# Performance work log

Measured on AMD Instinct MI355X. Metric: run time of the kernel, lower is better.

The kernel has to match this reference:

```python
import jax, jax.numpy as jnp
import numpy as np

N = 50000      # nodes
E = 600000     # edges (avg degree 12)
D_IN = 32      # Processor hard-codes first GBlock in_channels=32
D_H = 128      # args.d_hidden
N_MID = 3      # n_mp - 1 = layers after the first (2 skip + 1 no-skip)


def setup_inputs() -> dict:
    key = jax.random.key(0)
    ks = jax.random.split(key, 10)
    s_in = 1.0 / np.sqrt(D_IN)
    s_h = 1.0 / np.sqrt(D_H)
    return {
        "z": jax.random.normal(ks[0], (N, D_IN), jnp.float32),
        "edge_index": jax.random.randint(ks[1], (2, E), 0, N, dtype=jnp.int32),
        "edge_weight": jax.random.uniform(ks[2], (E,), jnp.float32),
        "batch": jnp.zeros((N,), jnp.int32),
        # first GBlock (32 -> 128)
        "W_rel0": jax.random.normal(ks[3], (D_H, D_IN), jnp.float32) * s_in,
        "b_rel0": jax.random.normal(ks[4], (D_H,), jnp.float32) * 0.01,
        "W_root0": jax.random.normal(ks[5], (D_H, D_IN), jnp.float32) * s_in,
        # remaining 3 GBlocks (128 -> 128), stacked
        "W_rel": jax.random.normal(ks[6], (N_MID, D_H, D_H), jnp.float32) * s_h,
        "b_rel": jax.random.normal(ks[7], (N_MID, D_H), jnp.float32) * 0.01,
        "W_root": jax.random.normal(ks[8], (N_MID, D_H, D_H), jnp.float32) * s_h,
    }


def graph_conv(x, src, dst, w, W_rel, b_rel, W_root):
    # PyG GraphConv: lin_rel(sum_{j->i} w_e * x_j) + lin_root(x)
    msg = x[src] * w[:, None]                                   # [E, d] gather
    agg = jax.ops.segment_sum(msg, dst, num_segments=x.shape[0])  # [N, d] scatter-add
    return agg @ W_rel.T + b_rel + x @ W_root.T


def reference(z, edge_index, edge_weight, batch, W_rel0, b_rel0, W_root0, W_rel, b_rel, W_root):
    src, dst = edge_index[0], edge_index[1]
    # GBlock 0: 32 -> 128, norm=Identity, no skip
    out = jax.nn.relu(graph_conv(z, src, dst, edge_weight, W_rel0, b_rel0, W_root0))
    # GBlocks 1..2 with residual+relu, GBlock 3 without
    skips = (True, True, False)
    for i, skip in enumerate(skips):
        h = jax.nn.relu(graph_conv(out, src, dst, edge_weight, W_rel[i], b_rel[i], W_root[i]))
        out = jax.nn.relu(h + out) if skip else h
    # dropout with p=0.0 (eval) is identity
    return out
```

## Files before the change

### kernel.cpp

```cpp
#include <hip/hip_runtime.h>

#define N_NODES 50000
#define N_EDGES 600000
#define D_IN 32
#define D_H 128
#define CAP 64

typedef __attribute__((ext_vector_type(8))) short short8;
typedef __attribute__((ext_vector_type(4))) float f32x4;

static inline int cdiv(int a, int b) { return (a + b - 1) / b; }

__device__ inline unsigned short f2bf(float f) {
    unsigned int b = __float_as_uint(f);
    return (unsigned short)((b + 0x7FFFu + ((b >> 16) & 1u)) >> 16);
}
__device__ inline unsigned int pack_bf16(float a, float b) {
    return (unsigned int)f2bf(a) | ((unsigned int)f2bf(b) << 16);
}
__device__ inline float bf_lo(unsigned int u) { return __uint_as_float(u << 16); }
__device__ inline float bf_hi(unsigned int u) { return __uint_as_float(u & 0xFFFF0000u); }


__global__ __launch_bounds__(256) void prep_kernel(
    const float* __restrict__ z, unsigned int* __restrict__ zbf,
    const float* __restrict__ Wrel0, const float* __restrict__ Wroot0,
    const float* __restrict__ Wrel, const float* __restrict__ Wroot,
    unsigned short* __restrict__ W0, unsigned short* __restrict__ W1,
    int* __restrict__ cnt) {
    int i = blockIdx.x * 256 + threadIdx.x;
    if (i < N_NODES) cnt[i] = 0;
    if (i < N_NODES * D_IN / 4) {
        float4 v = ((const float4*)z)[i];
        ((uint2*)zbf)[i] = make_uint2(pack_bf16(v.x, v.y), pack_bf16(v.z, v.w));
    }
    if (i < 128 * 64) {
        int o = i >> 6, k = i & 63;
        float v = (k < 32) ? Wrel0[o * 32 + k] : Wroot0[o * 32 + (k - 32)];
        W0[i] = f2bf(v);
    }
    if (i < 3 * 128 * 256) {
        int L = i >> 15;
        int r = i & 32767;
        int o = r >> 8, k = r & 255;
        float v = (k < 128) ? Wrel[L * 16384 + o * 128 + k]
                            : Wroot[L * 16384 + o * 128 + (k - 128)];
        W1[i] = f2bf(v);
    }
}


__global__ void fillpad_kernel(const int* __restrict__ src, const int* __restrict__ dst,
                               const float* __restrict__ w, int* __restrict__ cnt,
                               int2* __restrict__ ep, int e) {
    int i = blockIdx.x * blockDim.x + threadIdx.x;
    if (i < e) {
        int d = dst[i];
        int slot = atomicAdd(&cnt[d], 1);
        if (slot < CAP) ep[(size_t)d * CAP + slot] = make_int2(src[i], __float_as_int(w[i]));
    }
}


__global__ __launch_bounds__(256) void agg128_kernel(
    const unsigned int* __restrict__ xbf, const int* __restrict__ cnt,
    const int2* __restrict__ ep, unsigned int* __restrict__ aggbf, int n) {
    int tid = threadIdx.x;
    int wid = tid >> 6, l = tid & 63;
    int sub = l >> 4, q = l & 15;
    int node = blockIdx.x * 16 + wid * 4 + sub;
    if (node >= n) return;
    int deg = cnt[node]; if (deg > CAP) deg = CAP;
    const uint4* X4 = (const uint4*)xbf;
    const unsigned long long* row = (const unsigned long long*)(ep + (size_t)node * CAP);
    float a0 = 0.f, a1 = 0.f, a2 = 0.f, a3 = 0.f, a4 = 0.f, a5 = 0.f, a6 = 0.f, a7 = 0.f;
    int j = 0;
    for (; j + 4 <= deg; j += 4) {
        unsigned long long e0 = __builtin_nontemporal_load(row + j);
        unsigned long long e1 = __builtin_nontemporal_load(row + j + 1);
        unsigned long long e2 = __builtin_nontemporal_load(row + j + 2);
        unsigned long long e3 = __builtin_nontemporal_load(row + j + 3);
        uint4 v0 = X4[(size_t)(unsigned int)e0 * 16 + q];
        uint4 v1 = X4[(size_t)(unsigned int)e1 * 16 + q];
        uint4 v2 = X4[(size_t)(unsigned int)e2 * 16 + q];
        uint4 v3 = X4[(size_t)(unsigned int)e3 * 16 + q];
        float w0 = __uint_as_float((unsigned int)(e0 >> 32));
        float w1 = __uint_as_float((unsigned int)(e1 >> 32));
        float w2 = __uint_as_float((unsigned int)(e2 >> 32));
        float w3 = __uint_as_float((unsigned int)(e3 >> 32));
        a0 += bf_lo(v0.x) * w0; a1 += bf_hi(v0.x) * w0; a2 += bf_lo(v0.y) * w0; a3 += bf_hi(v0.y) * w0;
        a4 += bf_lo(v0.z) * w0; a5 += bf_hi(v0.z) * w0; a6 += bf_lo(v0.w) * w0; a7 += bf_hi(v0.w) * w0;
        a0 += bf_lo(v1.x) * w1; a1 += bf_hi(v1.x) * w1; a2 += bf_lo(v1.y) * w1; a3 += bf_hi(v1.y) * w1;
        a4 += bf_lo(v1.z) * w1; a5 += bf_hi(v1.z) * w1; a6 += bf_lo(v1.w) * w1; a7 += bf_hi(v1.w) * w1;
        a0 += bf_lo(v2.x) * w2; a1 += bf_hi(v2.x) * w2; a2 += bf_lo(v2.y) * w2; a3 += bf_hi(v2.y) * w2;
        a4 += bf_lo(v2.z) * w2; a5 += bf_hi(v2.z) * w2; a6 += bf_lo(v2.w) * w2; a7 += bf_hi(v2.w) * w2;
        a0 += bf_lo(v3.x) * w3; a1 += bf_hi(v3.x) * w3; a2 += bf_lo(v3.y) * w3; a3 += bf_hi(v3.y) * w3;
        a4 += bf_lo(v3.z) * w3; a5 += bf_hi(v3.z) * w3; a6 += bf_lo(v3.w) * w3; a7 += bf_hi(v3.w) * w3;
    }
    for (; j < deg; j++) {
        unsigned long long e0 = __builtin_nontemporal_load(row + j);
        uint4 v0 = X4[(size_t)(unsigned int)e0 * 16 + q];
        float w0 = __uint_as_float((unsigned int)(e0 >> 32));
        a0 += bf_lo(v0.x) * w0; a1 += bf_hi(v0.x) * w0; a2 += bf_lo(v0.y) * w0; a3 += bf_hi(v0.y) * w0;
        a4 += bf_lo(v0.z) * w0; a5 += bf_hi(v0.z) * w0; a6 += bf_lo(v0.w) * w0; a7 += bf_hi(v0.w) * w0;
    }
    ((uint4*)aggbf)[(size_t)node * 16 + q] =
        make_uint4(pack_bf16(a0, a1), pack_bf16(a2, a3), pack_bf16(a4, a5), pack_bf16(a6, a7));
}

__global__ __launch_bounds__(256) void agg32_kernel(
    const unsigned int* __restrict__ zbf, const int* __restrict__ cnt,
    const int2* __restrict__ ep, unsigned int* __restrict__ aggbf, int n) {
    int tid = threadIdx.x;
    int wid = tid >> 6, l = tid & 63;
    int sub = l >> 4, q = l & 15;
    int node = blockIdx.x * 16 + wid * 4 + sub;
    if (node >= n) return;
    int deg = cnt[node]; if (deg > CAP) deg = CAP;
    const unsigned long long* row = (const unsigned long long*)(ep + (size_t)node * CAP);
    float a0 = 0.f, a1 = 0.f;
    int j = 0;
    for (; j + 4 <= deg; j += 4) {
        unsigned long long e0 = __builtin_nontemporal_load(row + j);
        unsigned long long e1 = __builtin_nontemporal_load(row + j + 1);
        unsigned long long e2 = __builtin_nontemporal_load(row + j + 2);
        unsigned long long e3 = __builtin_nontemporal_load(row + j + 3);
        unsigned int v0 = zbf[(size_t)(unsigned int)e0 * 16 + q];
        unsigned int v1 = zbf[(size_t)(unsigned int)e1 * 16 + q];
        unsigned int v2 = zbf[(size_t)(unsigned int)e2 * 16 + q];
        unsigned int v3 = zbf[(size_t)(unsigned int)e3 * 16 + q];
        float w0 = __uint_as_float((unsigned int)(e0 >> 32));
        float w1 = __uint_as_float((unsigned int)(e1 >> 32));
        float w2 = __uint_as_float((unsigned int)(e2 >> 32));
        float w3 = __uint_as_float((unsigned int)(e3 >> 32));
        a0 += bf_lo(v0) * w0; a1 += bf_hi(v0) * w0;
        a0 += bf_lo(v1) * w1; a1 += bf_hi(v1) * w1;
        a0 += bf_lo(v2) * w2; a1 += bf_hi(v2) * w2;
        a0 += bf_lo(v3) * w3; a1 += bf_hi(v3) * w3;
    }
    for (; j < deg; j++) {
        unsigned long long e0 = __builtin_nontemporal_load(row + j);
        unsigned int v0 = zbf[(size_t)(unsigned int)e0 * 16 + q];
        float w0 = __uint_as_float((unsigned int)(e0 >> 32));
        a0 += bf_lo(v0) * w0; a1 += bf_hi(v0) * w0;
    }
    aggbf[(size_t)node * 16 + q] = pack_bf16(a0, a1);
}


template <int KH, bool SKIP, bool FINAL>
__global__ __launch_bounds__(256) void lin_kernel(
    const unsigned short* __restrict__ agg, const unsigned short* __restrict__ x,
    const unsigned short* __restrict__ W2, const float* __restrict__ bias,
    void* __restrict__ outv, int n) {
    constexpr int K2 = 2 * KH;
    constexpr int NKS = K2 / 32;
    constexpr int LOGNKS = (NKS == 2) ? 1 : 3;
    constexpr int SLOTS = 16 * K2;
    __shared__ uint2 Abuf[SLOTS];
    const int tid = threadIdx.x;
    const int n0 = blockIdx.x * 64;

#pragma unroll
    for (int it = 0; it < SLOTS / 256; it++) {
        int d = tid + it * 256;
        int jh = d & 1;
        int l = (d >> 1) & 63;
        int ks = (d >> 7) & (NKS - 1);
        int mt = d >> (7 + LOGNKS);
        int r = mt * 16 + (l & 15);
        int k = ks * 32 + ((l >> 4) << 3) + jh * 4;
        int node = n0 + r;
        uint2 v = make_uint2(0u, 0u);
        if (node < n) {
            v = (k < KH) ? *(const uint2*)(agg + (size_t)node * KH + k)
                         : *(const uint2*)(x + (size_t)node * KH + (k - KH));
        }
        Abuf[d] = v;
    }
    __syncthreads();

    const int w = tid >> 6, l = tid & 63;
    const int lo16 = l & 15, hi = l >> 4;

    f32x4 acc[4][2];
#pragma unroll
    for (int nt = 0; nt < 2; nt++) {
        float bv = bias[w * 32 + nt * 16 + lo16];
#pragma unroll
        for (int mt = 0; mt < 4; mt++) acc[mt][nt] = (f32x4){bv, bv, bv, bv};
    }

    const short8* Afr = (const short8*)Abuf;
#pragma unroll
    for (int ks = 0; ks < NKS; ks++) {
        short8 bfr[2];
#pragma unroll
        for (int nt = 0; nt < 2; nt++) {
            int o = w * 32 + nt * 16 + lo16;
            bfr[nt] = *(const short8*)(W2 + (size_t)o * K2 + ks * 32 + hi * 8);
        }
#pragma unroll
        for (int mt = 0; mt < 4; mt++) {
            short8 afr = Afr[(mt * NKS + ks) * 64 + l];
            acc[mt][0] = __builtin_amdgcn_mfma_f32_16x16x32_bf16(afr, bfr[0], acc[mt][0], 0, 0, 0);
            acc[mt][1] = __builtin_amdgcn_mfma_f32_16x16x32_bf16(afr, bfr[1], acc[mt][1], 0, 0, 0);
        }
    }

    const unsigned short* Au16 = (const unsigned short*)Abuf;
#pragma unroll
    for (int mt = 0; mt < 4; mt++) {
#pragma unroll
        for (int j = 0; j < 4; j++) {
            int node = n0 + mt * 16 + hi * 4 + j;
            if (node < n) {
#pragma unroll
                for (int nt = 0; nt < 2; nt++) {
                    int o = w * 32 + nt * 16 + lo16;
                    float v = acc[mt][nt][j];
                    v = fmaxf(v, 0.f);
                    if (SKIP) {
                        int us = (((mt * NKS + 4 + w) * 64 + (nt * 2 + (lo16 >> 3)) * 16 + hi * 4 + j) * 2
                                  + ((lo16 >> 2) & 1)) * 4 + (lo16 & 3);
                        float xr = __uint_as_float((unsigned int)Au16[us] << 16);
                        v = fmaxf(v + xr, 0.f);
                    }
                    if (FINAL)
                        ((float*)outv)[(size_t)node * D_H + o] = v;
                    else
                        ((unsigned short*)outv)[(size_t)node * D_H + o] = f2bf(v);
                }
            }
        }
    }
}


extern "C" void kernel_launch(void* const* d_in, const int* in_sizes, int n_in,
                              void* d_out, int out_size, void* d_ws, size_t ws_size,
                              hipStream_t stream) {
    const float* z      = (const float*)d_in[0];
    const int*   eidx   = (const int*)d_in[1];
    const float* ew     = (const float*)d_in[2];
    const float* Wrel0  = (const float*)d_in[4];
    const float* brel0  = (const float*)d_in[5];
    const float* Wroot0 = (const float*)d_in[6];
    const float* Wrel   = (const float*)d_in[7];
    const float* brel   = (const float*)d_in[8];
    const float* Wroot  = (const float*)d_in[9];

    const int* src = eidx;
    const int* dst = eidx + N_EDGES;

    char* p = (char*)d_ws;
    auto alloc = [&](size_t bytes) {
        void* r = (void*)p;
        p += (bytes + 255) & ~(size_t)255;
        return r;
    };
    int*   cnt   = (int*)alloc((size_t)N_NODES * 4);
    int2*  epack = (int2*)alloc((size_t)N_NODES * CAP * 8);
    unsigned int* zbf = (unsigned int*)alloc((size_t)N_NODES * D_IN * 2);
    unsigned int* agg = (unsigned int*)alloc((size_t)N_NODES * D_H * 2);
    unsigned int* h0  = (unsigned int*)alloc((size_t)N_NODES * D_H * 2);
    unsigned int* h1  = (unsigned int*)alloc((size_t)N_NODES * D_H * 2);
    unsigned short* W0bf = (unsigned short*)alloc((size_t)128 * 64 * 2);
    unsigned short* W1bf = (unsigned short*)alloc((size_t)3 * 128 * 256 * 2);
    float* outp = (float*)d_out;

    prep_kernel<<<cdiv(N_NODES * D_IN / 4, 256), 256, 0, stream>>>(
        z, zbf, Wrel0, Wroot0, Wrel, Wroot, W0bf, W1bf, cnt);

    fillpad_kernel<<<cdiv(N_EDGES, 256), 256, 0, stream>>>(src, dst, ew, cnt, epack, N_EDGES);

    const int aggGrid = cdiv(N_NODES, 16);
    const int linGrid = cdiv(N_NODES, 64);

    agg32_kernel<<<aggGrid, 256, 0, stream>>>(zbf, cnt, epack, agg, N_NODES);
    lin_kernel<32, false, false><<<linGrid, 256, 0, stream>>>(
        (const unsigned short*)agg, (const unsigned short*)zbf, W0bf, brel0, h0, N_NODES);
    agg128_kernel<<<aggGrid, 256, 0, stream>>>(h0, cnt, epack, agg, N_NODES);
    lin_kernel<128, true, false><<<linGrid, 256, 0, stream>>>(
        (const unsigned short*)agg, (const unsigned short*)h0, W1bf, brel, h1, N_NODES);
    agg128_kernel<<<aggGrid, 256, 0, stream>>>(h1, cnt, epack, agg, N_NODES);
    lin_kernel<128, true, false><<<linGrid, 256, 0, stream>>>(
        (const unsigned short*)agg, (const unsigned short*)h1, W1bf + 32768, brel + 128, h0, N_NODES);
    agg128_kernel<<<aggGrid, 256, 0, stream>>>(h0, cnt, epack, agg, N_NODES);
    lin_kernel<128, false, true><<<linGrid, 256, 0, stream>>>(
        (const unsigned short*)agg, (const unsigned short*)h0, W1bf + 65536, brel + 256, outp, N_NODES);
}
```

Baseline: 201.9 us.

## Partition agg128 feature columns across XCDs for L2 locality of gathers

```diff
diff --git a/kernel.cpp b/kernel.cpp
--- a/kernel.cpp
+++ b/kernel.cpp
@@ -5,6 +5,7 @@
 #define D_IN 32
 #define D_H 128
 #define CAP 64
+#define GPC 391
 
 typedef __attribute__((ext_vector_type(8))) short short8;
 typedef __attribute__((ext_vector_type(4))) float f32x4;
@@ -65,13 +66,18 @@
 __global__ __launch_bounds__(256) void agg128_kernel(
     const unsigned int* __restrict__ xbf, const int* __restrict__ cnt,
     const int2* __restrict__ ep, unsigned int* __restrict__ aggbf, int n) {
+    int b = blockIdx.x;
+    int xcd = b & 7, g = b >> 3;
+    int chunk = xcd >> 1, half = xcd & 1;
+    int ng = half * GPC + g;
     int tid = threadIdx.x;
-    int wid = tid >> 6, l = tid & 63;
-    int sub = l >> 4, q = l & 15;
-    int node = blockIdx.x * 16 + wid * 4 + sub;
+    int w = tid >> 6, l = tid & 63;
+    int node = ng * 64 + w * 16 + (l >> 2);
+    int s = l & 3;
     if (node >= n) return;
     int deg = cnt[node]; if (deg > CAP) deg = CAP;
     const uint4* X4 = (const uint4*)xbf;
+    const int co = chunk * 4 + s;
     const unsigned long long* row = (const unsigned long long*)(ep + (size_t)node * CAP);
     float a0 = 0.f, a1 = 0.f, a2 = 0.f, a3 = 0.f, a4 = 0.f, a5 = 0.f, a6 = 0.f, a7 = 0.f;
     int j = 0;
@@ -80,10 +86,10 @@
         unsigned long long e1 = __builtin_nontemporal_load(row + j + 1);
         unsigned long long e2 = __builtin_nontemporal_load(row + j + 2);
         unsigned long long e3 = __builtin_nontemporal_load(row + j + 3);
-        uint4 v0 = X4[(size_t)(unsigned int)e0 * 16 + q];
-        uint4 v1 = X4[(size_t)(unsigned int)e1 * 16 + q];
-        uint4 v2 = X4[(size_t)(unsigned int)e2 * 16 + q];
-        uint4 v3 = X4[(size_t)(unsigned int)e3 * 16 + q];
+        uint4 v0 = X4[(size_t)(unsigned int)e0 * 16 + co];
+        uint4 v1 = X4[(size_t)(unsigned int)e1 * 16 + co];
+        uint4 v2 = X4[(size_t)(unsigned int)e2 * 16 + co];
+        uint4 v3 = X4[(size_t)(unsigned int)e3 * 16 + co];
         float w0 = __uint_as_float((unsigned int)(e0 >> 32));
         float w1 = __uint_as_float((unsigned int)(e1 >> 32));
         float w2 = __uint_as_float((unsigned int)(e2 >> 32));
@@ -99,12 +105,12 @@
     }
     for (; j < deg; j++) {
         unsigned long long e0 = __builtin_nontemporal_load(row + j);
-        uint4 v0 = X4[(size_t)(unsigned int)e0 * 16 + q];
+        uint4 v0 = X4[(size_t)(unsigned int)e0 * 16 + co];
         float w0 = __uint_as_float((unsigned int)(e0 >> 32));
         a0 += bf_lo(v0.x) * w0; a1 += bf_hi(v0.x) * w0; a2 += bf_lo(v0.y) * w0; a3 += bf_hi(v0.y) * w0;
         a4 += bf_lo(v0.z) * w0; a5 += bf_hi(v0.z) * w0; a6 += bf_lo(v0.w) * w0; a7 += bf_hi(v0.w) * w0;
     }
-    ((uint4*)aggbf)[(size_t)node * 16 + q] =
+    ((uint4*)aggbf)[(size_t)node * 16 + co] =
         make_uint4(pack_bf16(a0, a1), pack_bf16(a2, a3), pack_bf16(a4, a5), pack_bf16(a6, a7));
 }
 
@@ -274,19 +280,20 @@
 
     fillpad_kernel<<<cdiv(N_EDGES, 256), 256, 0, stream>>>(src, dst, ew, cnt, epack, N_EDGES);
 
-    const int aggGrid = cdiv(N_NODES, 16);
-    const int linGrid = cdiv(N_NODES, 64);
-
-    agg32_kernel<<<aggGrid, 256, 0, stream>>>(zbf, cnt, epack, agg, N_NODES);
+    const int agg128Grid = 8 * GPC;
+    const int agg32Grid  = cdiv(N_NODES, 16);
+    const int linGrid    = cdiv(N_NODES, 64);
+
+    agg32_kernel<<<agg32Grid, 256, 0, stream>>>(zbf, cnt, epack, agg, N_NODES);
     lin_kernel<32, false, false><<<linGrid, 256, 0, stream>>>(
         (const unsigned short*)agg, (const unsigned short*)zbf, W0bf, brel0, h0, N_NODES);
-    agg128_kernel<<<aggGrid, 256, 0, stream>>>(h0, cnt, epack, agg, N_NODES);
+    agg128_kernel<<<agg128Grid, 256, 0, stream>>>(h0, cnt, epack, agg, N_NODES);
     lin_kernel<128, true, false><<<linGrid, 256, 0, stream>>>(
         (const unsigned short*)agg, (const unsigned short*)h0, W1bf, brel, h1, N_NODES);
-    agg128_kernel<<<aggGrid, 256, 0, stream>>>(h1, cnt, epack, agg, N_NODES);
+    agg128_kernel<<<agg128Grid, 256, 0, stream>>>(h1, cnt, epack, agg, N_NODES);
     lin_kernel<128, true, false><<<linGrid, 256, 0, stream>>>(
         (const unsigned short*)agg, (const unsigned short*)h1, W1bf + 32768, brel + 128, h0, N_NODES);
-    agg128_kernel<<<aggGrid, 256, 0, stream>>>(h0, cnt, epack, agg, N_NODES);
+    agg128_kernel<<<agg128Grid, 256, 0, stream>>>(h0, cnt, epack, agg, N_NODES);
     lin_kernel<128, false, true><<<linGrid, 256, 0, stream>>>(
         (const unsigned short*)agg, (const unsigned short*)h0, W1bf + 65536, brel + 256, outp, N_NODES);
 }
```

Measured after the change: 258.9 us. 1.28x slower.
